# Kernel tuning notes

Measured on AMD Instinct MI355X. Metric: run time of the kernel, lower is better.

The kernel has to match this reference:

```python
import jax, jax.numpy as jnp
import numpy as np

V = 10000
B = 8
N = 2048

def setup_inputs() -> dict:
    key = jax.random.key(0)
    kw, kW, kr = jax.random.split(key, 3)
    words = jax.random.randint(kw, (B, N), 0, V)              # [B,N] token ids
    W = jax.random.normal(kW, (V, V), dtype=jnp.float32) * 0.02  # linear.weight [out,in]
    root = jax.random.normal(kr, (V,), dtype=jnp.float32)        # root param [V]
    return {"words": words, "W": W, "root": root}

def reference(words, W, root):
    # out = one_hot(words) @ I (frozen identity embedding), so
    # einsum('bnh,hg,bmg->bnm', out, W, out) == W[words_n, words_m]
    final = W[words[:, :, None], words[:, None, :]]  # [B,N,N] gather
    root_score = root[words]                          # [B,N]  einsum('bnh,h->bn')
    i = jnp.arange(words.shape[1])
    final = final.at[:, i, i].add(root_score)         # diagonal scatter-add
    return final
```

## Files before the change

### kernel.cpp

```cpp
#include <hip/hip_runtime.h>


#define VOCAB 10000
#define BATCH 8
#define SEQ   2048
#define TPB   512

__global__ __launch_bounds__(TPB) void gather2d_lds_kernel(
    const int*   __restrict__ words,
    const float* __restrict__ W,
    const float* __restrict__ root,
    float*       __restrict__ out)
{
    __shared__ float row[VOCAB];

    const int i = blockIdx.x;
    const int b = blockIdx.y;
    const int wi = words[b * SEQ + i];
    const float rs = root[wi];

    const float* __restrict__ Wrow = W + (size_t)wi * VOCAB;
    const int*   __restrict__ wrow = words + b * SEQ;
    float*       __restrict__ orow = out + ((size_t)b * SEQ + i) * SEQ;

    #pragma unroll
    for (int it = 0; it < 5; ++it) {
        const int idx = it * TPB + threadIdx.x;
        if (idx < VOCAB / 4) {
            __builtin_amdgcn_global_load_lds(
                (const __attribute__((address_space(1))) void*)(Wrow + idx * 4),
                (__attribute__((address_space(3))) void*)(row + idx * 4),
                16, 0, 0);
        }
    }
    __syncthreads();

    const int j = threadIdx.x * 4;
    const int4 wj = *(const int4*)(wrow + j);
    float4 v;
    v.x = row[wj.x];
    v.y = row[wj.y];
    v.z = row[wj.z];
    v.w = row[wj.w];
    const unsigned d = (unsigned)(i - j);
    if (d < 4u) ((float*)&v)[d] += rs;
    *(float4*)(orow + j) = v;
}

extern "C" void kernel_launch(void* const* d_in, const int* in_sizes, int n_in,
                              void* d_out, int out_size, void* d_ws, size_t ws_size,
                              hipStream_t stream)
{
    const int*   words = (const int*)d_in[0];
    const float* W     = (const float*)d_in[1];
    const float* root  = (const float*)d_in[2];
    float*       out   = (float*)d_out;

    dim3 grid(SEQ, BATCH);
    gather2d_lds_kernel<<<grid, TPB, 0, stream>>>(words, W, root, out);
}
```

Before: 580.0 us.

## Double-buffer W row staging across 16 rows per block

Each block now handles 16 consecutive output rows instead of one. It double-buffers the W row in LDS so the async global-to-LDS copy of the next row runs while the current row is gathered and stored. The next word ids and root values are also prefetched ahead of use. The aim is to hide global load latency and cut per-block launch and setup cost. The price is twice the LDS per block (about 80KB), which lowers occupancy, and the overlap depends on the compiler not inserting a full vmcnt wait before LDS reads.

```diff
diff --git a/kernel.cpp b/kernel.cpp
--- a/kernel.cpp
+++ b/kernel.cpp
@@ -1,50 +1,77 @@
 #include <hip/hip_runtime.h>
 
 
-#define VOCAB 10000
-#define BATCH 8
-#define SEQ   2048
-#define TPB   512
+#define VOCAB  10000
+#define BATCH  8
+#define SEQ    2048
+#define TPB    512
+#define RPB    16
+#define NROWS  (BATCH * SEQ)
+#define NBLK   (NROWS / RPB)
+#define NCHUNK (VOCAB / 4)
 
-__global__ __launch_bounds__(TPB) void gather2d_lds_kernel(
+__device__ __forceinline__ void stage_row(const float* __restrict__ src,
+                                          float* dst )
+{
+    #pragma unroll
+    for (int it = 0; it < 5; ++it) {
+        const int idx = it * TPB + (int)threadIdx.x;
+        if (idx < NCHUNK) {
+            __builtin_amdgcn_global_load_lds(
+                (const __attribute__((address_space(1))) void*)(src + idx * 4),
+                (__attribute__((address_space(3))) void*)(dst + idx * 4),
+                16, 0, 0);
+        }
+    }
+}
+
+__global__ __launch_bounds__(TPB) void gather2d_pipe_kernel(
     const int*   __restrict__ words,
     const float* __restrict__ W,
     const float* __restrict__ root,
     float*       __restrict__ out)
 {
-    __shared__ float row[VOCAB];
+    __shared__ float buf[2][VOCAB];
 
-    const int i = blockIdx.x;
-    const int b = blockIdx.y;
-    const int wi = words[b * SEQ + i];
-    const float rs = root[wi];
+    const int r0 = blockIdx.x * RPB;
+    const int b  = r0 / SEQ;
+    const int i0 = r0 % SEQ;
+    const int* __restrict__ wrow = words + b * SEQ;
+    float* __restrict__ obase = out + ((size_t)b * SEQ + i0) * SEQ;
 
-    const float* __restrict__ Wrow = W + (size_t)wi * VOCAB;
-    const int*   __restrict__ wrow = words + b * SEQ;
-    float*       __restrict__ orow = out + ((size_t)b * SEQ + i) * SEQ;
+    const int  j  = (int)threadIdx.x * 4;
+    const int4 wj = *(const int4*)(wrow + j);
+
+    int   wi_cur = wrow[i0];
+    int   wi_nxt = wrow[i0 + 1];
+    float rs_cur = root[wi_cur];
+
+    stage_row(W + (size_t)wi_cur * VOCAB, buf[0]);
 
     #pragma unroll
-    for (int it = 0; it < 5; ++it) {
-        const int idx = it * TPB + threadIdx.x;
-        if (idx < VOCAB / 4) {
-            __builtin_amdgcn_global_load_lds(
-                (const __attribute__((address_space(1))) void*)(Wrow + idx * 4),
-                (__attribute__((address_space(3))) void*)(row + idx * 4),
-                16, 0, 0);
-        }
+    for (int k = 0; k < RPB; ++k) {
+        __syncthreads();
+
+        if (k + 1 < RPB)
+            stage_row(W + (size_t)wi_nxt * VOCAB, buf[(k + 1) & 1]);
+
+        const int   wi_fut = wrow[i0 + ((k + 2 < RPB) ? (k + 2) : 0)];
+        const float rs_nxt = root[wi_nxt];
+
+        const float* __restrict__ rp = buf[k & 1];
+        float4 v;
+        v.x = rp[wj.x];
+        v.y = rp[wj.y];
+        v.z = rp[wj.z];
+        v.w = rp[wj.w];
+        const unsigned d = (unsigned)((i0 + k) - j);
+        if (d < 4u) ((float*)&v)[d] += rs_cur;
+        *(float4*)(obase + (size_t)k * SEQ + j) = v;
+
+        wi_cur = wi_nxt;
+        rs_cur = rs_nxt;
+        wi_nxt = wi_fut;
     }
-    __syncthreads();
-
-    const int j = threadIdx.x * 4;
-    const int4 wj = *(const int4*)(wrow + j);
-    float4 v;
-    v.x = row[wj.x];
-    v.y = row[wj.y];
-    v.z = row[wj.z];
-    v.w = row[wj.w];
-    const unsigned d = (unsigned)(i - j);
-    if (d < 4u) ((float*)&v)[d] += rs;
-    *(float4*)(orow + j) = v;
 }
 
 extern "C" void kernel_launch(void* const* d_in, const int* in_sizes, int n_in,
@@ -56,6 +83,6 @@
     const float* root  = (const float*)d_in[2];
     float*       out   = (float*)d_out;
 
-    dim3 grid(SEQ, BATCH);
-    gather2d_lds_kernel<<<grid, TPB, 0, stream>>>(words, W, root, out);
+    dim3 grid(NBLK);
+    gather2d_pipe_kernel<<<grid, TPB, 0, stream>>>(words, W, root, out);
 }
```

Result: no change. 580.8 us (+0.1%).
